# Optimization experiments

Measured on AMD Instinct MI355X. Metric: run time of the kernel, lower is better.

## Reference

```python
import jax, jax.numpy as jnp
import numpy as np

IN_CH = 128
HID = 256   # 2 * out_channels
OUT_CH = 128
N_NODES = 10000
N_EDGES = 640000


def setup_inputs() -> dict:
    key = jax.random.key(0)
    ks = jax.random.split(key, 6)
    x = jax.random.normal(ks[0], (N_NODES, IN_CH), dtype=jnp.float32)
    edge_index = jax.random.randint(ks[1], (2, N_EDGES), 0, N_NODES, dtype=jnp.int64)
    # GCNConv params (glorot-like scale)
    W1 = jax.random.normal(ks[2], (IN_CH, HID), dtype=jnp.float32) / np.sqrt(IN_CH)
    b1 = jnp.zeros((HID,), dtype=jnp.float32)
    W2 = jax.random.normal(ks[3], (HID, OUT_CH), dtype=jnp.float32) / np.sqrt(HID)
    b2 = jnp.zeros((OUT_CH,), dtype=jnp.float32)
    return {"x": x, "edge_index": edge_index, "W1": W1, "b1": b1, "W2": W2, "b2": b2}


def _gcn_norm(edge_index, n_nodes):
    """Add self-loops and compute symmetric GCN normalization per edge."""
    loops = jnp.arange(n_nodes, dtype=edge_index.dtype)
    src = jnp.concatenate([edge_index[0], loops])  # [E+N]
    dst = jnp.concatenate([edge_index[1], loops])
    deg = jax.ops.segment_sum(jnp.ones_like(dst, dtype=jnp.float32), dst,
                              num_segments=n_nodes)
    dinv = jnp.where(deg > 0, jax.lax.rsqrt(deg), 0.0)
    norm = dinv[src] * dinv[dst]  # [E+N]
    return src, dst, norm


def _gcn_layer(x, W, b, src, dst, norm, n_nodes):
    h = x @ W                                  # [N, F_out]
    msg = h[src] * norm[:, None]               # gather + scale, [E+N, F_out]
    agg = jax.ops.segment_sum(msg, dst, num_segments=n_nodes)
    return agg + b


def reference(x, edge_index, W1, b1, W2, b2):
    n = x.shape[0]
    src, dst, norm = _gcn_norm(edge_index, n)
    h = jax.nn.relu(_gcn_layer(x, W1, b1, src, dst, norm, n))
    out = jax.nn.relu(_gcn_layer(h, W2, b2, src, dst, norm, n))
    return out
```

## Files before the change

### kernel.cpp

```cpp
#include <hip/hip_runtime.h>

#define N_FEAT 128
#define HID 256
#define OUT_CH 128

#define NB 256
#define MAXN 10240
#define CH 16
#define CB (NB / CH)

__device__ __forceinline__ unsigned bf16rn(float f) {
    unsigned u = __float_as_uint(f);
    return (u + 0x7fffu + ((u >> 16) & 1u)) >> 16;
}
__device__ __forceinline__ unsigned pack_bf16x2(float lo, float hi) {
    return bf16rn(lo) | (bf16rn(hi) << 16);
}
__device__ __forceinline__ float2 unpack_bf16x2(unsigned u) {
    float2 r;
    r.x = __uint_as_float(u << 16);
    r.y = __uint_as_float(u & 0xffff0000u);
    return r;
}


__global__ __launch_bounds__(256)
void hist_kernel(const int* __restrict__ dst, unsigned short* __restrict__ bh,
                 int E, int N, int chunk) {
    __shared__ int hist[MAXN];
    for (int i = threadIdx.x; i < N; i += 256) hist[i] = 0;
    __syncthreads();
    int base = blockIdx.x * chunk;
    int lim = min(chunk, E - base);
    for (int i = threadIdx.x; i < lim; i += 256) {
        int d = dst[base + i];
        if (d >= 0 && d < N) atomicAdd(&hist[d], 1);
    }
    __syncthreads();
    unsigned short* out = bh + (size_t)blockIdx.x * N;
    for (int i = threadIdx.x; i < N; i += 256) out[i] = (unsigned short)hist[i];
}

__global__ __launch_bounds__(256)
void colscan_kernel(const unsigned short* __restrict__ bh,
                    int* __restrict__ ps, int* __restrict__ counts,
                    float* __restrict__ dinv, int N) {
    int j = blockIdx.x * 256 + threadIdx.x;
    if (j >= N) return;
    int run = 0;
    for (int c = 0; c < CH; c++) {
        int s = 0;
        #pragma unroll
        for (int b = c * CB; b < (c + 1) * CB; b++) s += bh[(size_t)b * N + j];
        ps[(size_t)c * N + j] = run;
        run += s;
    }
    counts[j] = run;
    dinv[j] = rsqrtf((float)(run + 1));
}

#define SCAN_T 1024
#define SCAN_MAX_PER 16
__global__ __launch_bounds__(SCAN_T)
void scan_kernel(const int* __restrict__ counts,
                 int* __restrict__ row_start, int n) {
    int tid = threadIdx.x;
    int per = (n + SCAN_T - 1) / SCAN_T;
    int base = tid * per;
    int local[SCAN_MAX_PER];
    int sum = 0;
    for (int j = 0; j < per; j++) {
        int i = base + j;
        int c = (i < n) ? counts[i] : 0;
        local[j] = sum;
        sum += c;
    }
    int lane = tid & 63;
    int wave = tid >> 6;
    int incl = sum;
    #pragma unroll
    for (int off = 1; off < 64; off <<= 1) {
        int t = __shfl_up(incl, off, 64);
        if (lane >= off) incl += t;
    }
    __shared__ int wsum[16];
    __shared__ int woff[16];
    if (lane == 63) wsum[wave] = incl;
    __syncthreads();
    if (wave == 0) {
        int w = (lane < 16) ? wsum[lane] : 0;
        int v = w;
        #pragma unroll
        for (int off = 1; off < 16; off <<= 1) {
            int t = __shfl_up(v, off, 64);
            if (lane >= off) v += t;
        }
        if (lane < 16) woff[lane] = v - w;
    }
    __syncthreads();
    int thread_excl = woff[wave] + (incl - sum);
    for (int j = 0; j < per; j++) {
        int i = base + j;
        if (i < n) row_start[i] = thread_excl + local[j];
    }
    if (tid == SCAN_T - 1) row_start[n] = thread_excl + sum;
}

__global__ __launch_bounds__(256)
void chunkbase_kernel(unsigned short* __restrict__ bh,
                      const int* __restrict__ ps, int N) {
    int j = blockIdx.x * 256 + threadIdx.x;
    if (j >= N) return;
    int c = blockIdx.y;
    int run = ps[(size_t)c * N + j];
    #pragma unroll
    for (int b = c * CB; b < (c + 1) * CB; b++) {
        size_t idx = (size_t)b * N + j;
        int t = bh[idx];
        bh[idx] = (unsigned short)run;
        run += t;
    }
}

__global__ __launch_bounds__(256)
void scat_kernel(const int* __restrict__ src, const int* __restrict__ dst,
                 const unsigned short* __restrict__ bh,
                 const int* __restrict__ row_start,
                 int* __restrict__ csr_src, int E, int N, int chunk) {
    __shared__ int cur[MAXN];
    const unsigned short* basep = bh + (size_t)blockIdx.x * N;
    for (int i = threadIdx.x; i < N; i += 256)
        cur[i] = row_start[i] + (int)basep[i];
    __syncthreads();
    int base = blockIdx.x * chunk;
    int lim = min(chunk, E - base);
    for (int i = threadIdx.x; i < lim; i += 256) {
        int e = base + i;
        int d = dst[e];
        if (d < 0 || d >= N) continue;
        int pos = atomicAdd(&cur[d], 1);
        if ((unsigned)pos < (unsigned)E) csr_src[pos] = src[e];
    }
}

__global__ void prescale_kernel(const float* __restrict__ x,
                                const float* __restrict__ dinv,
                                unsigned* __restrict__ xs_b, int total4) {
    int i = blockIdx.x * blockDim.x + threadIdx.x;
    if (i < total4) {
        int row = i >> 5;
        float d = dinv[row];
        float4 v = ((const float4*)x)[i];
        uint2 p;
        p.x = pack_bf16x2(v.x * d, v.y * d);
        p.y = pack_bf16x2(v.z * d, v.w * d);
        ((uint2*)xs_b)[i] = p;
    }
}

template <bool EPILOGUE>
__global__ __launch_bounds__(256)
void agg_kernel(const unsigned* __restrict__ featb,
                const float* __restrict__ dinv,
                const int* __restrict__ row_start,
                const int* __restrict__ csr_src,
                const float* __restrict__ bias,
                float* __restrict__ out, int N) {
    int wave = threadIdx.x >> 6;
    int n = blockIdx.x * 4 + wave;
    if (n >= N) return;
    int f = threadIdx.x & 63;
    float dn = dinv[n];
    float2 v = unpack_bf16x2(featb[(size_t)n * 64 + f]);
    float accx = v.x;
    float accy = v.y;
    int e0 = row_start[n];
    int e1 = row_start[n + 1];
    int e = e0;
    for (; e + 16 <= e1; e += 16) {
        int s[16];
        #pragma unroll
        for (int j = 0; j < 16; j++) s[j] = csr_src[e + j];
        unsigned w[16];
        #pragma unroll
        for (int j = 0; j < 16; j++) w[j] = featb[(size_t)s[j] * 64 + f];
        #pragma unroll
        for (int j = 0; j < 16; j++) {
            float2 u = unpack_bf16x2(w[j]);
            accx += u.x;
            accy += u.y;
        }
    }
    for (; e + 4 <= e1; e += 4) {
        int s0 = csr_src[e], s1 = csr_src[e + 1];
        int s2 = csr_src[e + 2], s3 = csr_src[e + 3];
        unsigned w0 = featb[(size_t)s0 * 64 + f];
        unsigned w1 = featb[(size_t)s1 * 64 + f];
        unsigned w2 = featb[(size_t)s2 * 64 + f];
        unsigned w3 = featb[(size_t)s3 * 64 + f];
        float2 u0 = unpack_bf16x2(w0), u1 = unpack_bf16x2(w1);
        float2 u2 = unpack_bf16x2(w2), u3 = unpack_bf16x2(w3);
        accx += u0.x + u1.x + u2.x + u3.x;
        accy += u0.y + u1.y + u2.y + u3.y;
    }
    for (; e < e1; ++e) {
        float2 u = unpack_bf16x2(featb[(size_t)csr_src[e] * 64 + f]);
        accx += u.x;
        accy += u.y;
    }
    accx *= dn;
    accy *= dn;
    if (EPILOGUE) {
        float2 b = ((const float2*)bias)[f];
        accx = fmaxf(accx + b.x, 0.0f);
        accy = fmaxf(accy + b.y, 0.0f);
    }
    float2 r;
    r.x = accx;
    r.y = accy;
    ((float2*)out)[(size_t)n * 64 + f] = r;
}

template <bool BIAS_RELU, bool RSCALE, bool BF16_OUT>
__global__ __launch_bounds__(256)
void gemm_kernel(const float* __restrict__ A,
                 const float* __restrict__ B,
                 const float* __restrict__ bias,
                 const float* __restrict__ rscale,
                 void* __restrict__ Cv, int M, int N, int K) {
    __shared__ float As[16][68];
    __shared__ float Bs[16][64];
    int tid = threadIdx.x;
    int n0 = blockIdx.x * 64;
    int m0 = blockIdx.y * 64;
    int tx = tid & 15;
    int ty = tid >> 4;
    int ar = tid >> 2;
    int akq = tid & 3;
    int bk = tid >> 4;
    int bnq = tid & 15;
    float acc[4][4] = {};
    for (int k0 = 0; k0 < K; k0 += 16) {
        float4 av = make_float4(0.f, 0.f, 0.f, 0.f);
        if (m0 + ar < M)
            av = *(const float4*)&A[(size_t)(m0 + ar) * K + k0 + akq * 4];
        float4 bv = *(const float4*)&B[(size_t)(k0 + bk) * N + n0 + bnq * 4];
        As[akq * 4 + 0][ar] = av.x;
        As[akq * 4 + 1][ar] = av.y;
        As[akq * 4 + 2][ar] = av.z;
        As[akq * 4 + 3][ar] = av.w;
        *(float4*)&Bs[bk][bnq * 4] = bv;
        __syncthreads();
        #pragma unroll
        for (int k = 0; k < 16; k++) {
            float4 ra = *(const float4*)&As[k][ty * 4];
            float4 rb = *(const float4*)&Bs[k][tx * 4];
            acc[0][0] = fmaf(ra.x, rb.x, acc[0][0]);
            acc[0][1] = fmaf(ra.x, rb.y, acc[0][1]);
            acc[0][2] = fmaf(ra.x, rb.z, acc[0][2]);
            acc[0][3] = fmaf(ra.x, rb.w, acc[0][3]);
            acc[1][0] = fmaf(ra.y, rb.x, acc[1][0]);
            acc[1][1] = fmaf(ra.y, rb.y, acc[1][1]);
            acc[1][2] = fmaf(ra.y, rb.z, acc[1][2]);
            acc[1][3] = fmaf(ra.y, rb.w, acc[1][3]);
            acc[2][0] = fmaf(ra.z, rb.x, acc[2][0]);
            acc[2][1] = fmaf(ra.z, rb.y, acc[2][1]);
            acc[2][2] = fmaf(ra.z, rb.z, acc[2][2]);
            acc[2][3] = fmaf(ra.z, rb.w, acc[2][3]);
            acc[3][0] = fmaf(ra.w, rb.x, acc[3][0]);
            acc[3][1] = fmaf(ra.w, rb.y, acc[3][1]);
            acc[3][2] = fmaf(ra.w, rb.z, acc[3][2]);
            acc[3][3] = fmaf(ra.w, rb.w, acc[3][3]);
        }
        __syncthreads();
    }
    #pragma unroll
    for (int i = 0; i < 4; i++) {
        int m = m0 + ty * 4 + i;
        if (m >= M) continue;
        float rs = RSCALE ? rscale[m] : 1.0f;
        float v[4];
        #pragma unroll
        for (int j = 0; j < 4; j++) {
            v[j] = acc[i][j];
            if (RSCALE) v[j] *= rs;
            if (BIAS_RELU) v[j] = fmaxf(v[j] + bias[n0 + tx * 4 + j], 0.0f);
        }
        if (BF16_OUT) {
            unsigned* Cb = (unsigned*)Cv;
            size_t base = (size_t)m * (N >> 1) + ((n0 + tx * 4) >> 1);
            Cb[base] = pack_bf16x2(v[0], v[1]);
            Cb[base + 1] = pack_bf16x2(v[2], v[3]);
        } else {
            float* C = (float*)Cv;
            #pragma unroll
            for (int j = 0; j < 4; j++)
                C[(size_t)m * N + n0 + tx * 4 + j] = v[j];
        }
    }
}


static inline size_t align512(size_t x) { return (x + 511) & ~(size_t)511; }

extern "C" void kernel_launch(void* const* d_in, const int* in_sizes, int n_in,
                              void* d_out, int out_size, void* d_ws, size_t ws_size,
                              hipStream_t stream) {
    const float* x = (const float*)d_in[0];
    const int* ei = (const int*)d_in[1];
    const float* W1 = (const float*)d_in[2];
    const float* b1 = (const float*)d_in[3];
    const float* W2 = (const float*)d_in[4];
    const float* b2 = (const float*)d_in[5];
    float* out = (float*)d_out;

    const int N = in_sizes[0] / N_FEAT;
    const int E = in_sizes[1] / 2;
    const int* src = ei;
    const int* dst = ei + E;

    char* ws = (char*)d_ws;
    size_t off = 0;
    float* dinv = (float*)(ws + off);    off += align512((size_t)N * 4);
    int* counts = (int*)(ws + off);      off += align512((size_t)N * 4);
    int* row_start = (int*)(ws + off);   off += align512((size_t)(N + 1) * 4);
    int* csr_src = (int*)(ws + off);     off += align512((size_t)E * 4);
    unsigned* xs_b = (unsigned*)(ws + off); off += align512((size_t)N * 64 * 4);
    float* h = (float*)(ws + off);       off += align512((size_t)N * HID * 4);
    unsigned* t_b = (unsigned*)(ws + off); off += align512((size_t)N * 64 * 4);
    int* ps = (int*)(ws + off);          off += align512((size_t)CH * N * 4);
    unsigned short* bh = (unsigned short*)(ws + off);
    off += align512((size_t)NB * N * 2);
    (void)ws_size;
    float* agg1 = out;
    const int chunk = (E + NB - 1) / NB;
    const int NJ = (N + 255) / 256;

    hist_kernel<<<NB, 256, 0, stream>>>(dst, bh, E, N, chunk);
    colscan_kernel<<<NJ, 256, 0, stream>>>(bh, ps, counts, dinv, N);
    scan_kernel<<<1, SCAN_T, 0, stream>>>(counts, row_start, N);
    chunkbase_kernel<<<dim3(NJ, CH), 256, 0, stream>>>(bh, ps, N);
    scat_kernel<<<NB, 256, 0, stream>>>(src, dst, bh, row_start, csr_src, E, N, chunk);

    {
        int total4 = N * N_FEAT / 4;
        prescale_kernel<<<(total4 + 255) / 256, 256, 0, stream>>>(x, dinv, xs_b, total4);
    }

    agg_kernel<false><<<(N + 3) / 4, 256, 0, stream>>>(xs_b, dinv, row_start, csr_src,
                                                       nullptr, agg1, N);

    {
        dim3 grid(HID / 64, (N + 63) / 64);
        gemm_kernel<true, false, false><<<grid, 256, 0, stream>>>(
            agg1, W1, b1, nullptr, h, N, HID, N_FEAT);
    }

    {
        dim3 grid(OUT_CH / 64, (N + 63) / 64);
        gemm_kernel<false, true, true><<<grid, 256, 0, stream>>>(
            h, W2, nullptr, dinv, t_b, N, OUT_CH, HID);
    }

    agg_kernel<true><<<(N + 3) / 4, 256, 0, stream>>>(t_b, dinv, row_start, csr_src,
                                                      b2, out, N);
}
```

Measured before the change: 179.4 us.

## Fuse both dense GEMMs into one MLP kernel keeping hidden tile in LDS

Replaces the two separate GEMM launches (agg1@W1 with bias+ReLU, then h@W2 with row scaling) with a single kernel per 64-row block. The 64x256 hidden tile is stored in shared memory as bf16 instead of being written to and re-read from global memory as fp32. This removes one launch and the global round trip for h, but gives each block a larger register footprint (64 accumulators) and more LDS, and the grid shrinks to about 157 blocks. That lowers occupancy and parallelism on a GPU with many CUs, and rounding the hidden activations to bf16 before the second GEMM slightly changes numerics.

```diff
diff --git a/kernel.cpp b/kernel.cpp
--- a/kernel.cpp
+++ b/kernel.cpp
@@ -221,56 +221,123 @@
     ((float2*)out)[(size_t)n * 64 + f] = r;
 }
 
-template <bool BIAS_RELU, bool RSCALE, bool BF16_OUT>
-__global__ __launch_bounds__(256)
-void gemm_kernel(const float* __restrict__ A,
-                 const float* __restrict__ B,
-                 const float* __restrict__ bias,
-                 const float* __restrict__ rscale,
-                 void* __restrict__ Cv, int M, int N, int K) {
+__global__ __launch_bounds__(256)
+void mlp_kernel(const float* __restrict__ A,
+                const float* __restrict__ W1,
+                const float* __restrict__ b1,
+                const float* __restrict__ W2,
+                const float* __restrict__ dinv,
+                unsigned* __restrict__ Tb,
+                int M) {
     __shared__ float As[16][68];
-    __shared__ float Bs[16][64];
+    __shared__ float Ws[16][256];
+    __shared__ unsigned Hs[64][129];
     int tid = threadIdx.x;
-    int n0 = blockIdx.x * 64;
-    int m0 = blockIdx.y * 64;
+    int m0 = blockIdx.x * 64;
     int tx = tid & 15;
     int ty = tid >> 4;
     int ar = tid >> 2;
     int akq = tid & 3;
     int bk = tid >> 4;
     int bnq = tid & 15;
-    float acc[4][4] = {};
-    for (int k0 = 0; k0 < K; k0 += 16) {
+
+    float acc[4][4][4];
+    #pragma unroll
+    for (int i = 0; i < 4; i++)
+        #pragma unroll
+        for (int ct = 0; ct < 4; ct++)
+            #pragma unroll
+            for (int j = 0; j < 4; j++) acc[i][ct][j] = 0.0f;
+    for (int k0 = 0; k0 < N_FEAT; k0 += 16) {
         float4 av = make_float4(0.f, 0.f, 0.f, 0.f);
         if (m0 + ar < M)
-            av = *(const float4*)&A[(size_t)(m0 + ar) * K + k0 + akq * 4];
-        float4 bv = *(const float4*)&B[(size_t)(k0 + bk) * N + n0 + bnq * 4];
+            av = *(const float4*)&A[(size_t)(m0 + ar) * N_FEAT + k0 + akq * 4];
         As[akq * 4 + 0][ar] = av.x;
         As[akq * 4 + 1][ar] = av.y;
         As[akq * 4 + 2][ar] = av.z;
         As[akq * 4 + 3][ar] = av.w;
-        *(float4*)&Bs[bk][bnq * 4] = bv;
+        #pragma unroll
+        for (int i = 0; i < 4; i++)
+            *(float4*)&Ws[bk][bnq * 4 + 64 * i] =
+                *(const float4*)&W1[(size_t)(k0 + bk) * HID + bnq * 4 + 64 * i];
         __syncthreads();
         #pragma unroll
         for (int k = 0; k < 16; k++) {
             float4 ra = *(const float4*)&As[k][ty * 4];
-            float4 rb = *(const float4*)&Bs[k][tx * 4];
-            acc[0][0] = fmaf(ra.x, rb.x, acc[0][0]);
-            acc[0][1] = fmaf(ra.x, rb.y, acc[0][1]);
-            acc[0][2] = fmaf(ra.x, rb.z, acc[0][2]);
-            acc[0][3] = fmaf(ra.x, rb.w, acc[0][3]);
-            acc[1][0] = fmaf(ra.y, rb.x, acc[1][0]);
-            acc[1][1] = fmaf(ra.y, rb.y, acc[1][1]);
-            acc[1][2] = fmaf(ra.y, rb.z, acc[1][2]);
-            acc[1][3] = fmaf(ra.y, rb.w, acc[1][3]);
-            acc[2][0] = fmaf(ra.z, rb.x, acc[2][0]);
-            acc[2][1] = fmaf(ra.z, rb.y, acc[2][1]);
-            acc[2][2] = fmaf(ra.z, rb.z, acc[2][2]);
-            acc[2][3] = fmaf(ra.z, rb.w, acc[2][3]);
-            acc[3][0] = fmaf(ra.w, rb.x, acc[3][0]);
-            acc[3][1] = fmaf(ra.w, rb.y, acc[3][1]);
-            acc[3][2] = fmaf(ra.w, rb.z, acc[3][2]);
-            acc[3][3] = fmaf(ra.w, rb.w, acc[3][3]);
+            #pragma unroll
+            for (int ct = 0; ct < 4; ct++) {
+                float4 rb = *(const float4*)&Ws[k][tx * 4 + 64 * ct];
+                acc[0][ct][0] = fmaf(ra.x, rb.x, acc[0][ct][0]);
+                acc[0][ct][1] = fmaf(ra.x, rb.y, acc[0][ct][1]);
+                acc[0][ct][2] = fmaf(ra.x, rb.z, acc[0][ct][2]);
+                acc[0][ct][3] = fmaf(ra.x, rb.w, acc[0][ct][3]);
+                acc[1][ct][0] = fmaf(ra.y, rb.x, acc[1][ct][0]);
+                acc[1][ct][1] = fmaf(ra.y, rb.y, acc[1][ct][1]);
+                acc[1][ct][2] = fmaf(ra.y, rb.z, acc[1][ct][2]);
+                acc[1][ct][3] = fmaf(ra.y, rb.w, acc[1][ct][3]);
+                acc[2][ct][0] = fmaf(ra.z, rb.x, acc[2][ct][0]);
+                acc[2][ct][1] = fmaf(ra.z, rb.y, acc[2][ct][1]);
+                acc[2][ct][2] = fmaf(ra.z, rb.z, acc[2][ct][2]);
+                acc[2][ct][3] = fmaf(ra.z, rb.w, acc[2][ct][3]);
+                acc[3][ct][0] = fmaf(ra.w, rb.x, acc[3][ct][0]);
+                acc[3][ct][1] = fmaf(ra.w, rb.y, acc[3][ct][1]);
+                acc[3][ct][2] = fmaf(ra.w, rb.z, acc[3][ct][2]);
+                acc[3][ct][3] = fmaf(ra.w, rb.w, acc[3][ct][3]);
+            }
+        }
+        __syncthreads();
+    }
+    #pragma unroll
+    for (int i = 0; i < 4; i++) {
+        int m = ty * 4 + i;
+        #pragma unroll
+        for (int ct = 0; ct < 4; ct++) {
+            int n = tx * 4 + 64 * ct;
+            float v0 = fmaxf(acc[i][ct][0] + b1[n + 0], 0.0f);
+            float v1 = fmaxf(acc[i][ct][1] + b1[n + 1], 0.0f);
+            float v2 = fmaxf(acc[i][ct][2] + b1[n + 2], 0.0f);
+            float v3 = fmaxf(acc[i][ct][3] + b1[n + 3], 0.0f);
+            Hs[m][(n >> 1) + 0] = pack_bf16x2(v0, v1);
+            Hs[m][(n >> 1) + 1] = pack_bf16x2(v2, v3);
+        }
+    }
+    __syncthreads();
+
+    float acc2[4][2][4];
+    #pragma unroll
+    for (int i = 0; i < 4; i++)
+        #pragma unroll
+        for (int ct = 0; ct < 2; ct++)
+            #pragma unroll
+            for (int j = 0; j < 4; j++) acc2[i][ct][j] = 0.0f;
+    for (int k0 = 0; k0 < HID; k0 += 16) {
+        #pragma unroll
+        for (int i = 0; i < 2; i++)
+            *(float4*)&Ws[bk][bnq * 4 + 64 * i] =
+                *(const float4*)&W2[(size_t)(k0 + bk) * OUT_CH + bnq * 4 + 64 * i];
+        __syncthreads();
+        #pragma unroll
+        for (int kp = 0; kp < 8; kp++) {
+            float2 hv[4];
+            #pragma unroll
+            for (int i = 0; i < 4; i++)
+                hv[i] = unpack_bf16x2(Hs[ty * 4 + i][(k0 >> 1) + kp]);
+            #pragma unroll
+            for (int s = 0; s < 2; s++) {
+                int k = kp * 2 + s;
+                #pragma unroll
+                for (int ct = 0; ct < 2; ct++) {
+                    float4 rb = *(const float4*)&Ws[k][tx * 4 + 64 * ct];
+                    #pragma unroll
+                    for (int i = 0; i < 4; i++) {
+                        float a = s ? hv[i].y : hv[i].x;
+                        acc2[i][ct][0] = fmaf(a, rb.x, acc2[i][ct][0]);
+                        acc2[i][ct][1] = fmaf(a, rb.y, acc2[i][ct][1]);
+                        acc2[i][ct][2] = fmaf(a, rb.z, acc2[i][ct][2]);
+                        acc2[i][ct][3] = fmaf(a, rb.w, acc2[i][ct][3]);
+                    }
+                }
+            }
         }
         __syncthreads();
     }
@@ -278,24 +345,16 @@
     for (int i = 0; i < 4; i++) {
         int m = m0 + ty * 4 + i;
         if (m >= M) continue;
-        float rs = RSCALE ? rscale[m] : 1.0f;
-        float v[4];
-        #pragma unroll
-        for (int j = 0; j < 4; j++) {
-            v[j] = acc[i][j];
-            if (RSCALE) v[j] *= rs;
-            if (BIAS_RELU) v[j] = fmaxf(v[j] + bias[n0 + tx * 4 + j], 0.0f);
-        }
-        if (BF16_OUT) {
-            unsigned* Cb = (unsigned*)Cv;
-            size_t base = (size_t)m * (N >> 1) + ((n0 + tx * 4) >> 1);
-            Cb[base] = pack_bf16x2(v[0], v[1]);
-            Cb[base + 1] = pack_bf16x2(v[2], v[3]);
-        } else {
-            float* C = (float*)Cv;
-            #pragma unroll
-            for (int j = 0; j < 4; j++)
-                C[(size_t)m * N + n0 + tx * 4 + j] = v[j];
+        float rs = dinv[m];
+        #pragma unroll
+        for (int ct = 0; ct < 2; ct++) {
+            int n = tx * 4 + 64 * ct;
+            float v0 = acc2[i][ct][0] * rs;
+            float v1 = acc2[i][ct][1] * rs;
+            float v2 = acc2[i][ct][2] * rs;
+            float v3 = acc2[i][ct][3] * rs;
+            Tb[(size_t)m * 64 + (n >> 1) + 0] = pack_bf16x2(v0, v1);
+            Tb[(size_t)m * 64 + (n >> 1) + 1] = pack_bf16x2(v2, v3);
         }
     }
 }
@@ -326,7 +385,6 @@
     int* row_start = (int*)(ws + off);   off += align512((size_t)(N + 1) * 4);
     int* csr_src = (int*)(ws + off);     off += align512((size_t)E * 4);
     unsigned* xs_b = (unsigned*)(ws + off); off += align512((size_t)N * 64 * 4);
-    float* h = (float*)(ws + off);       off += align512((size_t)N * HID * 4);
     unsigned* t_b = (unsigned*)(ws + off); off += align512((size_t)N * 64 * 4);
     int* ps = (int*)(ws + off);          off += align512((size_t)CH * N * 4);
     unsigned short* bh = (unsigned short*)(ws + off);
@@ -350,17 +408,7 @@
     agg_kernel<false><<<(N + 3) / 4, 256, 0, stream>>>(xs_b, dinv, row_start, csr_src,
                                                        nullptr, agg1, N);
 
-    {
-        dim3 grid(HID / 64, (N + 63) / 64);
-        gemm_kernel<true, false, false><<<grid, 256, 0, stream>>>(
-            agg1, W1, b1, nullptr, h, N, HID, N_FEAT);
-    }
-
-    {
-        dim3 grid(OUT_CH / 64, (N + 63) / 64);
-        gemm_kernel<false, true, true><<<grid, 256, 0, stream>>>(
-            h, W2, nullptr, dinv, t_b, N, OUT_CH, HID);
-    }
+    mlp_kernel<<<(N + 63) / 64, 256, 0, stream>>>(agg1, W1, b1, W2, dinv, t_b, N);
 
     agg_kernel<true><<<(N + 3) / 4, 256, 0, stream>>>(t_b, dinv, row_start, csr_src,
                                                       b2, out, N);
```

Measured after the change: 189.3 us. +5.6%, slower.
